# Kernel tuning notes

Hardware: AMD Instinct MI355X
Metric: run time of the kernel (lower is better)

The kernel has to match this reference:

```python
import jax, jax.numpy as jnp
import numpy as np

B, LQ, LK, D = 32, 1024, 1024, 256

def setup_inputs() -> dict:
    key = jax.random.key(0)
    ks = jax.random.split(key, 7)
    return {
        "raw_query": jax.random.normal(ks[0], (B, LQ, D), dtype=jnp.float32),
        "raw_key": jax.random.normal(ks[1], (B, LK, D), dtype=jnp.float32),
        "raw_value": jax.random.normal(ks[2], (B, LK, D), dtype=jnp.float32),
        "value_mask": jax.random.randint(ks[3], (B, LQ), 0, 2, dtype=jnp.int32),
        "WQ": jax.random.normal(ks[4], (D, D), dtype=jnp.float32) * 0.05,
        "WK": jax.random.normal(ks[5], (D, D), dtype=jnp.float32) * 0.05,
        "WV": jax.random.normal(ks[6], (D, D), dtype=jnp.float32) * 0.05,
    }

def reference(raw_query, raw_key, raw_value, value_mask, WQ, WK, WV):
    # Projections: [B, L, D] @ [D, D]
    Q = raw_query @ WQ
    K = raw_key @ WK
    V = raw_value @ WV
    # Scores: [B, LQ, LK] (use_scale=False -> no 1/sqrt(d_k))
    att = jnp.einsum("bqd,bkd->bqk", Q, K)
    # Mask expanded on axis=2 -> zeroes entire query rows of scores (faithful to tf.where+zeros_like)
    att = jnp.where(value_mask[:, :, None] > 0, att, jnp.zeros((), dtype=att.dtype))
    att = jax.nn.softmax(att, axis=-1)
    # Output: [B, LQ, D]
    return jnp.einsum("bqk,bkd->bqd", att, V)
```

## Files before the change

### kernel.cpp

```cpp
#include <hip/hip_runtime.h>
#include <hip/hip_bf16.h>
#include <math.h>

#define B_ 32
#define L_ 1024
#define D_ 256

typedef _Float16 half8 __attribute__((ext_vector_type(8)));
typedef __fp16   fp16x2 __attribute__((ext_vector_type(2)));
typedef short    s16x8 __attribute__((ext_vector_type(8)));
typedef float    f32x4 __attribute__((ext_vector_type(4)));

typedef __attribute__((address_space(3))) unsigned int lds_u32;
typedef __attribute__((address_space(1))) unsigned int gbl_u32;

__device__ __forceinline__ void gl_lds16(const void* g, void* l) {
    __builtin_amdgcn_global_load_lds((gbl_u32*)g, (lds_u32*)l, 16, 0, 0);
}

__device__ __forceinline__ unsigned short f2bf(float x) {
    unsigned u = __float_as_uint(x);
    u += 0x7FFFu + ((u >> 16) & 1u);
    return (unsigned short)(u >> 16);
}

__device__ __forceinline__ unsigned short f2h(float x) {
    _Float16 h = (_Float16)x;
    unsigned short u;
    __builtin_memcpy(&u, &h, 2);
    return u;
}

__device__ __forceinline__ unsigned pkrtz(float a, float b) {
    fp16x2 v = __builtin_amdgcn_cvt_pkrtz(a, b);
    unsigned u;
    __builtin_memcpy(&u, &v, 4);
    return u;
}

__global__ __launch_bounds__(256) void wprep_kernel(
    const float* __restrict__ W0, const float* __restrict__ W1,
    const float* __restrict__ W2, unsigned short* __restrict__ Wt)
{
    const int z = blockIdx.z;
    const float* __restrict__ W = (z == 0) ? W0 : (z == 1) ? W1 : W2;
    __shared__ unsigned short T[64][72];
    const int k0 = blockIdx.x << 6, n0 = blockIdx.y << 6;
    const int t = threadIdx.x;
    const int r = t >> 2, c0 = (t & 3) << 4;
    #pragma unroll
    for (int j = 0; j < 16; j += 4) {
        float4 w4 = *(const float4*)(W + (size_t)(k0 + r) * 256 + n0 + c0 + j);
        T[c0 + j + 0][r] = f2h(w4.x);
        T[c0 + j + 1][r] = f2h(w4.y);
        T[c0 + j + 2][r] = f2h(w4.z);
        T[c0 + j + 3][r] = f2h(w4.w);
    }
    __syncthreads();
    const int n = t >> 2, kc = (t & 3) << 4;
    unsigned short* dst = Wt + ((size_t)z << 16) + (size_t)(n0 + n) * 256 + k0 + kc;
    *(uint4*)(dst + 0) = *(const uint4*)&T[n][kc + 0];
    *(uint4*)(dst + 8) = *(const uint4*)&T[n][kc + 8];
}

__global__ __launch_bounds__(1024, 4) void proj_mfma_kernel(
    const float* __restrict__ A0, const float* __restrict__ A1,
    const float* __restrict__ A2, const unsigned short* __restrict__ Wt,
    unsigned short* __restrict__ Qh, unsigned short* __restrict__ Kh,
    unsigned short* __restrict__ Vt)
{
    __shared__ unsigned short SMEM[49152];
    unsigned short* Asm = SMEM;
    unsigned short* Bsm = SMEM + 16384;

    const int fblk = blockIdx.x;
    const int xt = fblk & 255;
    const int z  = fblk >> 8;
    const int bm = xt << 7;

    const float* __restrict__ A = (z == 0) ? A0 : (z == 1) ? A1 : A2;
    const int t = threadIdx.x, lane = t & 63, w = t >> 6;
    const int wm = (w >> 2) << 5, wn = (w & 3) << 6;

    const float* __restrict__ Ag = A + (size_t)bm * 256;
    const unsigned short* __restrict__ Bg = Wt + ((size_t)z << 16);

    f32x4 acc[2][4];
    const f32x4 z4 = {0.f, 0.f, 0.f, 0.f};
    #pragma unroll
    for (int mi = 0; mi < 2; ++mi)
        #pragma unroll
        for (int ni = 0; ni < 4; ++ni) acc[mi][ni] = z4;

    const int ar = t >> 3, ac = t & 7;
    float4 aA[2], aB[2];

#define LOADA(itv, AR)                                                          \
    {                                                                           \
        const float* ap = Ag + (size_t)ar * 256 + ((itv) << 6) + (ac << 3);     \
        AR[0] = *(const float4*)ap;                                             \
        AR[1] = *(const float4*)(ap + 4);                                       \
    }
#define WRITEA(buf, AR)                                                         \
    {                                                                           \
        uint4 d;                                                                \
        d.x = pkrtz(AR[0].x, AR[0].y);                                          \
        d.y = pkrtz(AR[0].z, AR[0].w);                                          \
        d.z = pkrtz(AR[1].x, AR[1].y);                                          \
        d.w = pkrtz(AR[1].z, AR[1].w);                                          \
        int cs = ac ^ (ar & 7);                                                 \
        *(uint4*)&Asm[((buf) << 13) + (ar << 6) + (cs << 3)] = d;               \
    }

    auto stageB = [&](int buf, int it) {
        #pragma unroll
        for (int i = 0; i < 2; ++i) {
            int o = (i << 10) + t;
            int r = o >> 3, c = o & 7;
            int cs = c ^ (r & 7);
            gl_lds16(Bg + (size_t)r * 256 + (it << 6) + (cs << 3),
                     &Bsm[(buf << 14) + (o << 3)]);
        }
    };
    auto compute = [&](int buf) {
        #pragma unroll
        for (int kc = 0; kc < 2; ++kc) {
            half8 af[2], bfr[4];
            #pragma unroll
            for (int mi = 0; mi < 2; ++mi) {
                int m = wm + (mi << 4) + (lane & 15);
                int cs = ((kc << 2) + (lane >> 4)) ^ (m & 7);
                af[mi] = *(const half8*)&Asm[(buf << 13) + (m << 6) + (cs << 3)];
            }
            #pragma unroll
            for (int ni = 0; ni < 4; ++ni) {
                int n = wn + (ni << 4) + (lane & 15);
                int cs = ((kc << 2) + (lane >> 4)) ^ (n & 7);
                bfr[ni] = *(const half8*)&Bsm[(buf << 14) + (n << 6) + (cs << 3)];
            }
            #pragma unroll
            for (int mi = 0; mi < 2; ++mi)
                #pragma unroll
                for (int ni = 0; ni < 4; ++ni)
                    acc[mi][ni] = __builtin_amdgcn_mfma_f32_16x16x32_f16(
                        af[mi], bfr[ni], acc[mi][ni], 0, 0, 0);
        }
    };

    LOADA(0, aA);
    WRITEA(0, aA);
    stageB(0, 0);
    LOADA(1, aB);
    __syncthreads();

    LOADA(2, aA);
    WRITEA(1, aB);
    stageB(1, 1);
    compute(0);
    __syncthreads();
    LOADA(3, aB);
    WRITEA(0, aA);
    stageB(0, 2);
    compute(1);
    __syncthreads();
    WRITEA(1, aB);
    stageB(1, 3);
    compute(0);
    __syncthreads();
    compute(1);

#undef LOADA
#undef WRITEA

    if (z < 2) {
        unsigned short* __restrict__ C = (z == 0) ? Qh : Kh;
        __syncthreads();
        unsigned short (*Cs)[264] = (unsigned short(*)[264])SMEM;
        #pragma unroll
        for (int mi = 0; mi < 2; ++mi) {
            int q0l = wm + (mi << 4) + ((lane >> 4) << 2);
            #pragma unroll
            for (int ni = 0; ni < 4; ++ni) {
                int cl = wn + (ni << 4) + (lane & 15);
                #pragma unroll
                for (int r = 0; r < 4; ++r)
                    Cs[q0l + r][cl] = f2h(acc[mi][ni][r]);
            }
        }
        __syncthreads();
        #pragma unroll
        for (int i = 0; i < 4; ++i) {
            int o = (i << 10) + t;
            int r = o >> 5, c = o & 31;
            *(uint4*)(C + (size_t)(bm + r) * 256 + (c << 3)) =
                *(const uint4*)&Cs[r][c << 3];
        }
    } else {
        unsigned short (*Tt)[136] = (unsigned short(*)[136])SMEM;
        const int bb = bm >> 10, kin = bm & 1023;
        #pragma unroll
        for (int dh = 0; dh < 2; ++dh) {
            __syncthreads();
            if (((w & 3) >> 1) == dh) {
                #pragma unroll
                for (int mi = 0; mi < 2; ++mi) {
                    int m0 = wm + (mi << 4) + ((lane >> 4) << 2);
                    #pragma unroll
                    for (int ni = 0; ni < 4; ++ni) {
                        int nl = (wn & 127) + (ni << 4) + (lane & 15);
                        #pragma unroll
                        for (int r = 0; r < 4; ++r)
                            Tt[nl][m0 + r] = f2bf(acc[mi][ni][r]);
                    }
                }
            }
            __syncthreads();
            int dr = t >> 3, cq = t & 7;
            unsigned short* dst = Vt + ((size_t)bb * 256 + (dh << 7) + dr) * 1024
                                  + kin + (cq << 4);
            *(uint4*)(dst + 0) = *(const uint4*)&Tt[dr][(cq << 4) + 0];
            *(uint4*)(dst + 8) = *(const uint4*)&Tt[dr][(cq << 4) + 8];
        }
    }
}

__global__ __launch_bounds__(1024, 4) void fused_attn_kernel(
    const unsigned short* __restrict__ Qh, const unsigned short* __restrict__ Kh,
    const unsigned short* __restrict__ Vt, const int* __restrict__ mask,
    float* __restrict__ Out)
{
    __shared__ unsigned short Ks[2][16384];
    __shared__ unsigned short Vs[2][16384];
    __shared__ unsigned short Ps[128 * 64];
    float* lredp = (float*)Ps;

    const int f  = blockIdx.x;
    const int b  = (f & 7) + ((f >> 6) << 3);
    const int q0 = ((f >> 3) & 7) << 7;
    const size_t bL = (size_t)b * L_;
    const int t = threadIdx.x, lane = t & 63, w = t >> 6;
    const int wm_s = (w >> 1) << 4, wn_s = (w & 1) << 5;
    const int wm_v = (w >> 2) << 5, wn_v = (w & 3) << 6;

    const unsigned short* __restrict__ Kb = Kh + (bL << 8);
    const unsigned short* __restrict__ Vb = Vt + (bL << 8);

    auto stageK = [&](int buf, int kt) {
        #pragma unroll
        for (int i = 0; i < 2; ++i) {
            int o = (i << 10) + t;
            int r = o >> 5, c = o & 31;
            int cs = (c & 24) | ((c & 7) ^ (r & 7));
            gl_lds16(Kb + (size_t)((kt << 6) + r) * 256 + (cs << 3), &Ks[buf][o << 3]);
        }
    };
    auto stageV = [&](int buf, int kt) {
        #pragma unroll
        for (int i = 0; i < 2; ++i) {
            int o = (i << 10) + t;
            int d = o >> 3, c = o & 7;
            int cs = c ^ (d & 7);
            gl_lds16(Vb + ((size_t)d << 10) + (kt << 6) + (cs << 3), &Vs[buf][o << 3]);
        }
    };

    stageK(0, 0);
    stageV(0, 0);

    half8 qf[8];
    {
        int m = wm_s + (lane & 15);
        const unsigned short* qp = Qh + ((bL + q0 + m) << 8) + ((lane >> 4) << 3);
        #pragma unroll
        for (int kc = 0; kc < 8; ++kc)
            qf[kc] = *(const half8*)(qp + (kc << 5));
    }
    int mv[4];
    {
        int qrow = wm_s + ((lane >> 4) << 2);
        #pragma unroll
        for (int r = 0; r < 4; ++r) mv[r] = mask[bL + q0 + qrow + r];
    }

    f32x4 o_acc[2][4];
    const f32x4 z4 = {0.f, 0.f, 0.f, 0.f};
    #pragma unroll
    for (int mi = 0; mi < 2; ++mi)
        #pragma unroll
        for (int ni = 0; ni < 4; ++ni) o_acc[mi][ni] = z4;
    float lacc[4] = {};

    __syncthreads();

    for (int kt = 0; kt < 16; ++kt) {
        const int cur = kt & 1;
        if (kt < 15) stageV(cur ^ 1, kt + 1);

        f32x4 accs[2];
        accs[0] = z4; accs[1] = z4;
        #pragma unroll
        for (int kc = 0; kc < 8; ++kc) {
            int kb = (kc >> 1) << 6, cc = ((kc & 1) << 2) + (lane >> 4);
            int n0 = wn_s + (lane & 15);
            int n1 = n0 + 16;
            half8 bf0 = *(const half8*)&Ks[cur][(n0 << 8) + kb + ((cc ^ (n0 & 7)) << 3)];
            half8 bf1 = *(const half8*)&Ks[cur][(n1 << 8) + kb + ((cc ^ (n1 & 7)) << 3)];
            accs[0] = __builtin_amdgcn_mfma_f32_16x16x32_f16(qf[kc], bf0, accs[0], 0, 0, 0);
            accs[1] = __builtin_amdgcn_mfma_f32_16x16x32_f16(qf[kc], bf1, accs[1], 0, 0, 0);
        }

        {
            int qrow = wm_s + ((lane >> 4) << 2);
            #pragma unroll
            for (int ni = 0; ni < 2; ++ni) {
                int kl = wn_s + (ni << 4) + (lane & 15);
                #pragma unroll
                for (int r = 0; r < 4; ++r) {
                    int q = qrow + r;
                    float p = mv[r] ? __expf(accs[ni][r]) : 1.0f;
                    Ps[(q << 6) + ((((kl >> 3) ^ (q & 7)) << 3)) + (kl & 7)] = f2bf(p);
                    lacc[r] += p;
                }
            }
        }
        __syncthreads();

        if (kt < 15) stageK(cur ^ 1, kt + 1);

        #pragma unroll
        for (int kc2 = 0; kc2 < 2; ++kc2) {
            s16x8 pa[2], vb[4];
            int cc = (kc2 << 2) + (lane >> 4);
            #pragma unroll
            for (int mi = 0; mi < 2; ++mi) {
                int m = wm_v + (mi << 4) + (lane & 15);
                pa[mi] = *(const s16x8*)&Ps[(m << 6) + ((cc ^ (m & 7)) << 3)];
            }
            #pragma unroll
            for (int ni = 0; ni < 4; ++ni) {
                int n = wn_v + (ni << 4) + (lane & 15);
                vb[ni] = *(const s16x8*)&Vs[cur][(n << 6) + ((cc ^ (n & 7)) << 3)];
            }
            #pragma unroll
            for (int mi = 0; mi < 2; ++mi)
                #pragma unroll
                for (int ni = 0; ni < 4; ++ni)
                    o_acc[mi][ni] = __builtin_amdgcn_mfma_f32_16x16x32_bf16(
                        pa[mi], vb[ni], o_acc[mi][ni], 0, 0, 0);
        }
        __syncthreads();
    }

    #pragma unroll
    for (int r = 0; r < 4; ++r) {
        float v = lacc[r];
        v += __shfl_xor(v, 1);
        v += __shfl_xor(v, 2);
        v += __shfl_xor(v, 4);
        v += __shfl_xor(v, 8);
        if ((lane & 15) == 0)
            lredp[((wm_s + ((lane >> 4) << 2) + r) << 1) + (w & 1)] = v;
    }
    __syncthreads();

    #pragma unroll
    for (int mi = 0; mi < 2; ++mi) {
        #pragma unroll
        for (int rr = 0; rr < 4; ++rr) {
            int q = wm_v + (mi << 4) + ((lane >> 4) << 2) + rr;
            float inv = 1.0f / (lredp[q << 1] + lredp[(q << 1) + 1]);
            #pragma unroll
            for (int ni = 0; ni < 4; ++ni) {
                int d = wn_v + (ni << 4) + (lane & 15);
                Out[((bL + q0 + q) << 8) + d] = o_acc[mi][ni][rr] * inv;
            }
        }
    }
}

extern "C" void kernel_launch(void* const* d_in, const int* in_sizes, int n_in,
                              void* d_out, int out_size, void* d_ws, size_t ws_size,
                              hipStream_t stream) {
    const float* rq = (const float*)d_in[0];
    const float* rk = (const float*)d_in[1];
    const float* rv = (const float*)d_in[2];
    const int*   vm = (const int*)d_in[3];
    const float* WQ = (const float*)d_in[4];
    const float* WK = (const float*)d_in[5];
    const float* WV = (const float*)d_in[6];
    float* out = (float*)d_out;

    char* ws = (char*)d_ws;
    unsigned short* Qh = (unsigned short*)(ws);
    unsigned short* Kh = (unsigned short*)(ws + ((size_t)16 << 20));
    unsigned short* Vt = (unsigned short*)(ws + ((size_t)32 << 20));
    unsigned short* Wt = (unsigned short*)(ws + ((size_t)48 << 20));

    dim3 wg(4, 4, 3);
    wprep_kernel<<<wg, 256, 0, stream>>>(WQ, WK, WV, Wt);

    proj_mfma_kernel<<<768, 1024, 0, stream>>>(rq, rk, rv, Wt, Qh, Kh, Vt);

    fused_attn_kernel<<<256, 1024, 0, stream>>>(Qh, Kh, Vt, vm, out);
}
```

Measured before the change: 90.42 us.

## Stage fp32 A tiles via async LDS loads and use explicit vmcnt waits

In the projection kernel, the fp32 input tiles are now copied straight into LDS with async global_load_lds instead of going through registers with an fp16 pack, and the fp16 conversion moves to fragment-load time. LDS use grows to 128KB. In the attention kernel, the K prefetch moves earlier so it is issued together with V. All __syncthreads are replaced by raw barriers with explicit s_waitcnt vmcnt counts, so prefetches can stay in flight across barriers. This saves register staging and waits, but the larger LDS footprint may reduce occupancy, and hand-counted vmcnt values risk races.

New measurement: 91.77 us. About the same (+1.5%).

```diff
diff --git a/kernel.cpp b/kernel.cpp
--- a/kernel.cpp
+++ b/kernel.cpp
@@ -37,6 +37,10 @@
     __builtin_memcpy(&u, &v, 4);
     return u;
 }
+
+#define WAITVL(N) asm volatile("s_waitcnt vmcnt(" #N ") lgkmcnt(0)" ::: "memory")
+#define WAITV(N)  asm volatile("s_waitcnt vmcnt(" #N ")" ::: "memory")
+#define BARRIER()  do { __builtin_amdgcn_s_barrier(); __builtin_amdgcn_sched_barrier(0); } while (0)
 
 __global__ __launch_bounds__(256) void wprep_kernel(
     const float* __restrict__ W0, const float* __restrict__ W1,
@@ -69,9 +73,9 @@
     unsigned short* __restrict__ Qh, unsigned short* __restrict__ Kh,
     unsigned short* __restrict__ Vt)
 {
-    __shared__ unsigned short SMEM[49152];
-    unsigned short* Asm = SMEM;
-    unsigned short* Bsm = SMEM + 16384;
+    __shared__ __align__(16) unsigned char SMEMRAW[131072];
+    float*          Asm = (float*)SMEMRAW;
+    unsigned short* Bsm = (unsigned short*)(SMEMRAW + 65536);
 
     const int fblk = blockIdx.x;
     const int xt = fblk & 255;
@@ -92,26 +96,16 @@
         #pragma unroll
         for (int ni = 0; ni < 4; ++ni) acc[mi][ni] = z4;
 
-    const int ar = t >> 3, ac = t & 7;
-    float4 aA[2], aB[2];
-
-#define LOADA(itv, AR)                                                          \
-    {                                                                           \
-        const float* ap = Ag + (size_t)ar * 256 + ((itv) << 6) + (ac << 3);     \
-        AR[0] = *(const float4*)ap;                                             \
-        AR[1] = *(const float4*)(ap + 4);                                       \
-    }
-#define WRITEA(buf, AR)                                                         \
-    {                                                                           \
-        uint4 d;                                                                \
-        d.x = pkrtz(AR[0].x, AR[0].y);                                          \
-        d.y = pkrtz(AR[0].z, AR[0].w);                                          \
-        d.z = pkrtz(AR[1].x, AR[1].y);                                          \
-        d.w = pkrtz(AR[1].z, AR[1].w);                                          \
-        int cs = ac ^ (ar & 7);                                                 \
-        *(uint4*)&Asm[((buf) << 13) + (ar << 6) + (cs << 3)] = d;               \
-    }
-
+    auto stageA = [&](int buf, int it) {
+        #pragma unroll
+        for (int i = 0; i < 2; ++i) {
+            int o = (i << 10) + t;
+            int r = o >> 4, c = o & 15;
+            int cs = (c & 8) | ((c & 7) ^ (r & 7));
+            gl_lds16(Ag + (size_t)r * 256 + (it << 6) + (cs << 2),
+                     &Asm[(buf << 13) + (o << 2)]);
+        }
+    };
     auto stageB = [&](int buf, int it) {
         #pragma unroll
         for (int i = 0; i < 2; ++i) {
@@ -128,9 +122,16 @@
             half8 af[2], bfr[4];
             #pragma unroll
             for (int mi = 0; mi < 2; ++mi) {
-                int m = wm + (mi << 4) + (lane & 15);
-                int cs = ((kc << 2) + (lane >> 4)) ^ (m & 7);
-                af[mi] = *(const half8*)&Asm[(buf << 13) + (m << 6) + (cs << 3)];
+                int m  = wm + (mi << 4) + (lane & 15);
+                int g2 = (lane >> 4) << 1;
+                int cs0 = (kc << 3) | ( g2      ^ (m & 7));
+                int cs1 = (kc << 3) | ((g2 | 1) ^ (m & 7));
+                float4 lo = *(const float4*)&Asm[(buf << 13) + (m << 6) + (cs0 << 2)];
+                float4 hi = *(const float4*)&Asm[(buf << 13) + (m << 6) + (cs1 << 2)];
+                unsigned hh[4];
+                hh[0] = pkrtz(lo.x, lo.y); hh[1] = pkrtz(lo.z, lo.w);
+                hh[2] = pkrtz(hi.x, hi.y); hh[3] = pkrtz(hi.z, hi.w);
+                __builtin_memcpy(&af[mi], hh, 16);
             }
             #pragma unroll
             for (int ni = 0; ni < 4; ++ni) {
@@ -147,35 +148,28 @@
         }
     };
 
-    LOADA(0, aA);
-    WRITEA(0, aA);
-    stageB(0, 0);
-    LOADA(1, aB);
-    __syncthreads();
-
-    LOADA(2, aA);
-    WRITEA(1, aB);
-    stageB(1, 1);
+    stageA(0, 0); stageB(0, 0);
+    WAITVL(0); BARRIER();
+
+    stageA(1, 1); stageB(1, 1);
+    WAITVL(4); BARRIER();
     compute(0);
-    __syncthreads();
-    LOADA(3, aB);
-    WRITEA(0, aA);
-    stageB(0, 2);
+    BARRIER();
+    stageA(0, 2); stageB(0, 2);
+    WAITVL(4); BARRIER();
     compute(1);
-    __syncthreads();
-    WRITEA(1, aB);
-    stageB(1, 3);
+    BARRIER();
+    stageA(1, 3); stageB(1, 3);
+    WAITVL(4); BARRIER();
     compute(0);
-    __syncthreads();
+    BARRIER();
+    WAITVL(0); BARRIER();
     compute(1);
-
-#undef LOADA
-#undef WRITEA
 
     if (z < 2) {
         unsigned short* __restrict__ C = (z == 0) ? Qh : Kh;
         __syncthreads();
-        unsigned short (*Cs)[264] = (unsigned short(*)[264])SMEM;
+        unsigned short (*Cs)[264] = (unsigned short(*)[264])SMEMRAW;
         #pragma unroll
         for (int mi = 0; mi < 2; ++mi) {
             int q0l = wm + (mi << 4) + ((lane >> 4) << 2);
@@ -196,7 +190,7 @@
                 *(const uint4*)&Cs[r][c << 3];
         }
     } else {
-        unsigned short (*Tt)[136] = (unsigned short(*)[136])SMEM;
+        unsigned short (*Tt)[136] = (unsigned short(*)[136])SMEMRAW;
         const int bb = bm >> 10, kin = bm & 1023;
         #pragma unroll
         for (int dh = 0; dh < 2; ++dh) {
@@ -247,6 +241,8 @@
 
     auto stageK = [&](int buf, int kt) {
         #pragma unroll
+        for (int i = 0; i < 1; ++i) { }
+        #pragma unroll
         for (int i = 0; i < 2; ++i) {
             int o = (i << 10) + t;
             int r = o >> 5, c = o & 31;
@@ -264,9 +260,6 @@
         }
     };
 
-    stageK(0, 0);
-    stageV(0, 0);
-
     half8 qf[8];
     {
         int m = wm_s + (lane & 15);
@@ -281,6 +274,8 @@
         #pragma unroll
         for (int r = 0; r < 4; ++r) mv[r] = mask[bL + q0 + qrow + r];
     }
+    stageK(0, 0);
+    stageV(0, 0);
 
     f32x4 o_acc[2][4];
     const f32x4 z4 = {0.f, 0.f, 0.f, 0.f};
@@ -290,11 +285,14 @@
         for (int ni = 0; ni < 4; ++ni) o_acc[mi][ni] = z4;
     float lacc[4] = {};
 
-    __syncthreads();
+    WAITVL(0); BARRIER();
 
     for (int kt = 0; kt < 16; ++kt) {
         const int cur = kt & 1;
-        if (kt < 15) stageV(cur ^ 1, kt + 1);
+        if (kt < 15) {
+            stageK(cur ^ 1, kt + 1);
+            stageV(cur ^ 1, kt + 1);
+        }
 
         f32x4 accs[2];
         accs[0] = z4; accs[1] = z4;
@@ -323,9 +321,8 @@
                 }
             }
         }
-        __syncthreads();
-
-        if (kt < 15) stageK(cur ^ 1, kt + 1);
+        if (kt < 15) { WAITVL(4); } else { WAITVL(0); }
+        BARRIER();
 
         #pragma unroll
         for (int kc2 = 0; kc2 < 2; ++kc2) {
@@ -348,7 +345,8 @@
                     o_acc[mi][ni] = __builtin_amdgcn_mfma_f32_16x16x32_bf16(
                         pa[mi], vb[ni], o_acc[mi][ni], 0, 0, 0);
         }
-        __syncthreads();
+        if (kt < 15) { WAITV(2); }
+        BARRIER();
     }
 
     #pragma unroll
```
